# Kernel optimization log

Measured on AMD Instinct MI355X. Metric: run time of the kernel, lower is better.

The kernel has to match this reference:

```python
import jax, jax.numpy as jnp
import numpy as np

EPS = 1e-8  # torch F.cosine_similarity default eps


def setup_inputs() -> dict:
    key = jax.random.key(0)
    k1, k2, k3, k4 = jax.random.split(key, 4)
    U, I, L = 8192, 8192, 256
    # xavier_uniform bound for Embedding weight (fan_in=n, fan_out=L)
    bu = float(np.sqrt(6.0 / (U + L)))
    bi = float(np.sqrt(6.0 / (I + L)))
    user_embed_w = jax.random.uniform(k1, (U, L), jnp.float32, -bu, bu)
    item_embed_w = jax.random.uniform(k2, (I, L), jnp.float32, -bi, bi)
    user_idx = jax.random.randint(k3, (1024,), 0, U, dtype=jnp.int64 if jax.config.jax_enable_x64 else jnp.int32)
    item_idx = jax.random.randint(k4, (1024,), 0, I, dtype=jnp.int64 if jax.config.jax_enable_x64 else jnp.int32)
    return {
        "user_embed_w": user_embed_w,
        "item_embed_w": item_embed_w,
        "user_idx": user_idx,
        "item_idx": item_idx,
        "is_test": 1,
    }


def _cosine_full(u, v):
    # Faithful to F.cosine_similarity(u[:,None], v[None,:], dim=-1) but
    # expressed as normalize + GEMM: (u.v) / (max(|u|,eps)*max(|v|,eps)).
    un = u / jnp.maximum(jnp.linalg.norm(u, axis=-1, keepdims=True), EPS)
    vn = v / jnp.maximum(jnp.linalg.norm(v, axis=-1, keepdims=True), EPS)
    return jnp.einsum("ul,il->ui", un, vn)  # [U, I]


def reference(user_embed_w, item_embed_w, user_idx, item_idx, is_test):
    if is_test:
        return _cosine_full(user_embed_w, item_embed_w)
    # training path: per-pair cosine similarity of user embeddings (note:
    # original code looks up BOTH indices in user_embed, faithfully kept)
    a = user_embed_w[user_idx]
    b = user_embed_w[item_idx]
    num = jnp.sum(a * b, axis=-1)
    den = jnp.maximum(jnp.linalg.norm(a, axis=-1), EPS) * jnp.maximum(
        jnp.linalg.norm(b, axis=-1), EPS
    )
    return (num / den).reshape(-1, 1)
```

## Files before the change

kernel.cpp:

```cpp
#include <hip/hip_runtime.h>
#include <hip/hip_bf16.h>
#include <stdint.h>


#define LDIM 256
#define NROWS 8192
#define NDIM 8192
#define BM 128
#define BN 128
#define BK 64

typedef __bf16 bf16x8 __attribute__((ext_vector_type(8)));
typedef float f32x4 __attribute__((ext_vector_type(4)));

__device__ __forceinline__ unsigned short f2bf_rne(float f) {
  union { float f; uint32_t u; } c;
  c.f = f;
  uint32_t u = c.u;
  u += 0x7FFFu + ((u >> 16) & 1u);
  return (unsigned short)(u >> 16);
}

__global__ __launch_bounds__(256) void normalize_both(
    const float* __restrict__ userw, const float* __restrict__ itemw,
    unsigned short* __restrict__ dst) {
  const int wave = threadIdx.x >> 6;
  const int lane = threadIdx.x & 63;
  const int row = blockIdx.x * 4 + wave;
  const float* src = (row < NROWS)
                         ? userw + (size_t)row * LDIM
                         : itemw + (size_t)(row - NROWS) * LDIM;

  const float4 v = reinterpret_cast<const float4*>(src)[lane];
  float ss = v.x * v.x + v.y * v.y + v.z * v.z + v.w * v.w;
#pragma unroll
  for (int off = 32; off; off >>= 1) ss += __shfl_xor(ss, off, 64);
  const float rn = 1.0f / fmaxf(sqrtf(ss), 1e-8f);

  ushort4 o;
  o.x = f2bf_rne(v.x * rn);
  o.y = f2bf_rne(v.y * rn);
  o.z = f2bf_rne(v.z * rn);
  o.w = f2bf_rne(v.w * rn);
  reinterpret_cast<ushort4*>(dst + (size_t)row * LDIM)[lane] = o;
}

__device__ __forceinline__ void gld_lds16(const __bf16* g, __bf16* l) {
  __builtin_amdgcn_global_load_lds(
      (const __attribute__((address_space(1))) uint32_t*)g,
      (__attribute__((address_space(3))) uint32_t*)l, 16, 0, 0);
}

__global__ __launch_bounds__(256) void cos_gemm(
    const __bf16* __restrict__ A, const __bf16* __restrict__ B,
    float* __restrict__ C) {
  __shared__ __align__(16) __bf16 As[2][BM * BK];
  __shared__ __align__(16) __bf16 Bs[2][BN * BK];

  const int tid = threadIdx.x;
  const int wid = tid >> 6;
  const int lane = tid & 63;
  const int bn = blockIdx.x, bm = blockIdx.y;
  const int wr = wid >> 1, wc = wid & 1;

  const int srow = tid >> 3;
  const int scbx = (((tid & 7) ^ (srow & 7)) << 4);
  const __bf16* gA = A + (size_t)(bm * BM + srow) * LDIM + (scbx >> 1);
  const __bf16* gB = B + (size_t)(bn * BN + srow) * LDIM + (scbx >> 1);

  const int fr = lane & 15;
  const int q = lane >> 4;
  const int rsw = (fr & 7) << 4;

  f32x4 acc[4][4] = {};

#define STAGE(buf, kt)                                                       \
  {                                                                          \
    _Pragma("unroll") for (int c = 0; c < 4; ++c) {                          \
      gld_lds16(gA + (size_t)(c * 32) * LDIM + (kt)*BK,                      \
                &As[buf][c * 2048 + wid * 512]);                             \
      gld_lds16(gB + (size_t)(c * 32) * LDIM + (kt)*BK,                      \
                &Bs[buf][c * 2048 + wid * 512]);                             \
    }                                                                        \
  }

#define COMPUTE(buf)                                                         \
  {                                                                          \
    _Pragma("unroll") for (int ks = 0; ks < 2; ++ks) {                       \
      bf16x8 af[4], bv[4];                                                   \
      const int kb = ((((ks << 6) | (q << 4)) ^ rsw) >> 1);                  \
      _Pragma("unroll") for (int m = 0; m < 4; ++m)                          \
          af[m] = *reinterpret_cast<const bf16x8*>(                          \
              &As[buf][(wr * 64 + m * 16 + fr) * BK + kb]);                  \
      _Pragma("unroll") for (int n = 0; n < 4; ++n)                          \
          bv[n] = *reinterpret_cast<const bf16x8*>(                          \
              &Bs[buf][(wc * 64 + n * 16 + fr) * BK + kb]);                  \
      _Pragma("unroll") for (int m = 0; m < 4; ++m)                          \
          _Pragma("unroll") for (int n = 0; n < 4; ++n)                      \
              acc[m][n] = __builtin_amdgcn_mfma_f32_16x16x32_bf16(           \
                  bv[n], af[m], acc[m][n], 0, 0, 0);                         \
    }                                                                        \
  }

  STAGE(0, 0);
  __syncthreads();
#pragma unroll
  for (int kt = 0; kt < 3; ++kt) {
    STAGE((kt + 1) & 1, kt + 1);
    COMPUTE(kt & 1);
    __syncthreads();
  }
  COMPUTE(1);

  float* Cp = C + (size_t)(bm * BM + wr * 64 + fr) * NDIM +
              (bn * BN + wc * 64 + (q << 2));
#pragma unroll
  for (int m = 0; m < 4; ++m)
#pragma unroll
    for (int n = 0; n < 4; ++n)
      *reinterpret_cast<f32x4*>(Cp + (size_t)(m * 16) * NDIM + n * 16) =
          acc[m][n];
#undef STAGE
#undef COMPUTE
}

extern "C" void kernel_launch(void* const* d_in, const int* in_sizes, int n_in,
                              void* d_out, int out_size, void* d_ws, size_t ws_size,
                              hipStream_t stream) {
  const float* user_w = (const float*)d_in[0];
  const float* item_w = (const float*)d_in[1];
  float* out = (float*)d_out;

  unsigned short* un = (unsigned short*)d_ws;
  unsigned short* vn = un + (size_t)NROWS * LDIM;

  normalize_both<<<(2 * NROWS) / 4, 256, 0, stream>>>(user_w, item_w, un);

  dim3 grid(NDIM / BN, NDIM / BM);
  cos_gemm<<<grid, 256, 0, stream>>>((const __bf16*)un, (const __bf16*)vn, out);
}
```

Before: 82.88 us.

## Write normalized operands in MFMA fragment order and load directly to registers

The normalize kernel now stores bf16 rows in a pre-swizzled layout matching the 16x16x32 MFMA fragment order. The GEMM then drops LDS staging and barriers and loads fragments straight from global memory into registers with a two-deep register double buffer. This removes LDS traffic and sync overhead. In exchange, operand reuse within a block now depends on L1/L2 caching instead of shared memory, and vector register pressure goes up.

```diff
diff --git a/kernel.cpp b/kernel.cpp
--- a/kernel.cpp
+++ b/kernel.cpp
@@ -8,7 +8,6 @@
 #define NDIM 8192
 #define BM 128
 #define BN 128
-#define BK 64
 
 typedef __bf16 bf16x8 __attribute__((ext_vector_type(8)));
 typedef float f32x4 __attribute__((ext_vector_type(4)));
@@ -21,7 +20,7 @@
   return (unsigned short)(u >> 16);
 }
 
-__global__ __launch_bounds__(256) void normalize_both(
+__global__ __launch_bounds__(256) void normalize_frag(
     const float* __restrict__ userw, const float* __restrict__ itemw,
     unsigned short* __restrict__ dst) {
   const int wave = threadIdx.x >> 6;
@@ -42,76 +41,58 @@
   o.y = f2bf_rne(v.y * rn);
   o.z = f2bf_rne(v.z * rn);
   o.w = f2bf_rne(v.w * rn);
-  reinterpret_cast<ushort4*>(dst + (size_t)row * LDIM)[lane] = o;
-}
 
-__device__ __forceinline__ void gld_lds16(const __bf16* g, __bf16* l) {
-  __builtin_amdgcn_global_load_lds(
-      (const __attribute__((address_space(1))) uint32_t*)g,
-      (__attribute__((address_space(3))) uint32_t*)l, 16, 0, 0);
+  const size_t base = (row < NROWS ? 0 : (size_t)NROWS * LDIM) +
+                      (size_t)((row & 8191) >> 4) * 4096;
+  const size_t off = base + ((lane >> 3) << 9) + (((lane >> 1) & 3) << 7) +
+                     ((row & 15) << 3) + ((lane & 1) << 2);
+  *reinterpret_cast<ushort4*>(dst + off) = o;
 }
 
 __global__ __launch_bounds__(256) void cos_gemm(
     const __bf16* __restrict__ A, const __bf16* __restrict__ B,
     float* __restrict__ C) {
-  __shared__ __align__(16) __bf16 As[2][BM * BK];
-  __shared__ __align__(16) __bf16 Bs[2][BN * BK];
-
   const int tid = threadIdx.x;
   const int wid = tid >> 6;
   const int lane = tid & 63;
   const int bn = blockIdx.x, bm = blockIdx.y;
   const int wr = wid >> 1, wc = wid & 1;
 
-  const int srow = tid >> 3;
-  const int scbx = (((tid & 7) ^ (srow & 7)) << 4);
-  const __bf16* gA = A + (size_t)(bm * BM + srow) * LDIM + (scbx >> 1);
-  const __bf16* gB = B + (size_t)(bn * BN + srow) * LDIM + (scbx >> 1);
-
-  const int fr = lane & 15;
-  const int q = lane >> 4;
-  const int rsw = (fr & 7) << 4;
+  const bf16x8* pa =
+      reinterpret_cast<const bf16x8*>(A) + (size_t)(bm * 8 + wr * 4) * 512 + lane;
+  const bf16x8* pb =
+      reinterpret_cast<const bf16x8*>(B) + (size_t)(bn * 8 + wc * 4) * 512 + lane;
 
   f32x4 acc[4][4] = {};
+  bf16x8 a0[4], b0[4], a1[4], b1[4];
 
-#define STAGE(buf, kt)                                                       \
+#define LD(aa, bb, kt)                                                       \
   {                                                                          \
-    _Pragma("unroll") for (int c = 0; c < 4; ++c) {                          \
-      gld_lds16(gA + (size_t)(c * 32) * LDIM + (kt)*BK,                      \
-                &As[buf][c * 2048 + wid * 512]);                             \
-      gld_lds16(gB + (size_t)(c * 32) * LDIM + (kt)*BK,                      \
-                &Bs[buf][c * 2048 + wid * 512]);                             \
-    }                                                                        \
+    _Pragma("unroll") for (int m = 0; m < 4; ++m) aa[m] =                    \
+        pa[m * 512 + (kt)*64];                                               \
+    _Pragma("unroll") for (int n = 0; n < 4; ++n) bb[n] =                    \
+        pb[n * 512 + (kt)*64];                                               \
+  }
+#define STEP(aa, bb)                                                         \
+  {                                                                          \
+    _Pragma("unroll") for (int m = 0; m < 4; ++m)                            \
+        _Pragma("unroll") for (int n = 0; n < 4; ++n)                        \
+            acc[m][n] = __builtin_amdgcn_mfma_f32_16x16x32_bf16(             \
+                bb[n], aa[m], acc[m][n], 0, 0, 0);                           \
   }
 
-#define COMPUTE(buf)                                                         \
-  {                                                                          \
-    _Pragma("unroll") for (int ks = 0; ks < 2; ++ks) {                       \
-      bf16x8 af[4], bv[4];                                                   \
-      const int kb = ((((ks << 6) | (q << 4)) ^ rsw) >> 1);                  \
-      _Pragma("unroll") for (int m = 0; m < 4; ++m)                          \
-          af[m] = *reinterpret_cast<const bf16x8*>(                          \
-              &As[buf][(wr * 64 + m * 16 + fr) * BK + kb]);                  \
-      _Pragma("unroll") for (int n = 0; n < 4; ++n)                          \
-          bv[n] = *reinterpret_cast<const bf16x8*>(                          \
-              &Bs[buf][(wc * 64 + n * 16 + fr) * BK + kb]);                  \
-      _Pragma("unroll") for (int m = 0; m < 4; ++m)                          \
-          _Pragma("unroll") for (int n = 0; n < 4; ++n)                      \
-              acc[m][n] = __builtin_amdgcn_mfma_f32_16x16x32_bf16(           \
-                  bv[n], af[m], acc[m][n], 0, 0, 0);                         \
-    }                                                                        \
+  LD(a0, b0, 0);
+#pragma unroll
+  for (int kt = 0; kt < 8; kt += 2) {
+    if (kt + 1 < 8) LD(a1, b1, kt + 1);
+    STEP(a0, b0);
+    if (kt + 2 < 8) LD(a0, b0, kt + 2);
+    STEP(a1, b1);
   }
+#undef LD
+#undef STEP
 
-  STAGE(0, 0);
-  __syncthreads();
-#pragma unroll
-  for (int kt = 0; kt < 3; ++kt) {
-    STAGE((kt + 1) & 1, kt + 1);
-    COMPUTE(kt & 1);
-    __syncthreads();
-  }
-  COMPUTE(1);
-
+  const int fr = lane & 15, q = lane >> 4;
   float* Cp = C + (size_t)(bm * BM + wr * 64 + fr) * NDIM +
               (bn * BN + wc * 64 + (q << 2));
 #pragma unroll
@@ -120,8 +101,6 @@
     for (int n = 0; n < 4; ++n)
       *reinterpret_cast<f32x4*>(Cp + (size_t)(m * 16) * NDIM + n * 16) =
           acc[m][n];
-#undef STAGE
-#undef COMPUTE
 }
 
 extern "C" void kernel_launch(void* const* d_in, const int* in_sizes, int n_in,
@@ -134,7 +113,7 @@
   unsigned short* un = (unsigned short*)d_ws;
   unsigned short* vn = un + (size_t)NROWS * LDIM;
 
-  normalize_both<<<(2 * NROWS) / 4, 256, 0, stream>>>(user_w, item_w, un);
+  normalize_frag<<<(2 * NROWS) / 4, 256, 0, stream>>>(user_w, item_w, un);
 
   dim3 grid(NDIM / BN, NDIM / BM);
   cos_gemm<<<grid, 256, 0, stream>>>((const __bf16*)un, (const __bf16*)vn, out);
```

After: 92.48 us. 1.12x slower.

## Make GEMM blocks persistent over four N tiles with cross-tile prefetch pipeline

Applied to the files above, without the earlier changes.

Each block now computes four consecutive 128x128 output tiles along N, using BK=32 double-buffered stages. The first K-slice of the next tile is prefetched during the last slice of the current one, so stores overlap loads. Waits use explicit vmcnt counters instead of __syncthreads, and the grid drops to 1024 blocks. This cuts launch and prologue cost per tile and overlaps epilogue stores with loads. In exchange there are fewer blocks for the CUs, an unswizzled LDS layout with possible bank conflicts, and fragile hand-written vmcnt counts.

```diff
diff --git a/kernel.cpp b/kernel.cpp
--- a/kernel.cpp
+++ b/kernel.cpp
@@ -8,7 +8,8 @@
 #define NDIM 8192
 #define BM 128
 #define BN 128
-#define BK 64
+#define BK 32
+#define TPB 4
 
 typedef __bf16 bf16x8 __attribute__((ext_vector_type(8)));
 typedef float f32x4 __attribute__((ext_vector_type(4)));
@@ -54,72 +55,91 @@
 __global__ __launch_bounds__(256) void cos_gemm(
     const __bf16* __restrict__ A, const __bf16* __restrict__ B,
     float* __restrict__ C) {
-  __shared__ __align__(16) __bf16 As[2][BM * BK];
-  __shared__ __align__(16) __bf16 Bs[2][BN * BK];
+  __shared__ __bf16 As[2][BM * BK];
+  __shared__ __bf16 Bs[2][BN * BK];
 
   const int tid = threadIdx.x;
   const int wid = tid >> 6;
   const int lane = tid & 63;
-  const int bn = blockIdx.x, bm = blockIdx.y;
+  const int b = blockIdx.x;
+  const int bm = b >> 4;
+  const int bn0 = (b & 15) * TPB;
+
   const int wr = wid >> 1, wc = wid & 1;
 
-  const int srow = tid >> 3;
-  const int scbx = (((tid & 7) ^ (srow & 7)) << 4);
-  const __bf16* gA = A + (size_t)(bm * BM + srow) * LDIM + (scbx >> 1);
-  const __bf16* gB = B + (size_t)(bn * BN + srow) * LDIM + (scbx >> 1);
+  const int m0 = (wid << 5) + (lane >> 2);
+  const int k0 = (lane & 3) << 3;
+  const __bf16* gA = A + (size_t)(bm * BM + m0) * LDIM + k0;
+  const __bf16* gB = B + (size_t)(bn0 * BN + m0) * LDIM + k0;
 
   const int fr = lane & 15;
   const int q = lane >> 4;
-  const int rsw = (fr & 7) << 4;
+  const int kq = q << 3;
 
   f32x4 acc[4][4] = {};
 
-#define STAGE(buf, kt)                                                       \
+#define STAGE(buf, ko, gBp)                                                  \
   {                                                                          \
-    _Pragma("unroll") for (int c = 0; c < 4; ++c) {                          \
-      gld_lds16(gA + (size_t)(c * 32) * LDIM + (kt)*BK,                      \
-                &As[buf][c * 2048 + wid * 512]);                             \
-      gld_lds16(gB + (size_t)(c * 32) * LDIM + (kt)*BK,                      \
-                &Bs[buf][c * 2048 + wid * 512]);                             \
+    _Pragma("unroll") for (int c = 0; c < 2; ++c) {                          \
+      gld_lds16(gA + (size_t)(c * 16) * LDIM + (ko),                         \
+                &As[buf][(wid << 10) + (c << 9)]);                           \
+      gld_lds16((gBp) + (size_t)(c * 16) * LDIM + (ko),                      \
+                &Bs[buf][(wid << 10) + (c << 9)]);                           \
     }                                                                        \
   }
 
 #define COMPUTE(buf)                                                         \
   {                                                                          \
-    _Pragma("unroll") for (int ks = 0; ks < 2; ++ks) {                       \
-      bf16x8 af[4], bv[4];                                                   \
-      const int kb = ((((ks << 6) | (q << 4)) ^ rsw) >> 1);                  \
-      _Pragma("unroll") for (int m = 0; m < 4; ++m)                          \
-          af[m] = *reinterpret_cast<const bf16x8*>(                          \
-              &As[buf][(wr * 64 + m * 16 + fr) * BK + kb]);                  \
-      _Pragma("unroll") for (int n = 0; n < 4; ++n)                          \
-          bv[n] = *reinterpret_cast<const bf16x8*>(                          \
-              &Bs[buf][(wc * 64 + n * 16 + fr) * BK + kb]);                  \
-      _Pragma("unroll") for (int m = 0; m < 4; ++m)                          \
-          _Pragma("unroll") for (int n = 0; n < 4; ++n)                      \
-              acc[m][n] = __builtin_amdgcn_mfma_f32_16x16x32_bf16(           \
-                  bv[n], af[m], acc[m][n], 0, 0, 0);                         \
-    }                                                                        \
+    bf16x8 af[4], bv[4];                                                     \
+    _Pragma("unroll") for (int m = 0; m < 4; ++m)                            \
+        af[m] = *reinterpret_cast<const bf16x8*>(                            \
+            &As[buf][(wr * 64 + m * 16 + fr) * BK + kq]);                    \
+    _Pragma("unroll") for (int n = 0; n < 4; ++n)                            \
+        bv[n] = *reinterpret_cast<const bf16x8*>(                            \
+            &Bs[buf][(wc * 64 + n * 16 + fr) * BK + kq]);                    \
+    _Pragma("unroll") for (int m = 0; m < 4; ++m)                            \
+        _Pragma("unroll") for (int n = 0; n < 4; ++n)                        \
+            acc[m][n] = __builtin_amdgcn_mfma_f32_16x16x32_bf16(             \
+                bv[n], af[m], acc[m][n], 0, 0, 0);                           \
   }
 
-  STAGE(0, 0);
-  __syncthreads();
+  STAGE(0, 0, gB);
+  float* Cp = C + (size_t)(bm * BM + wr * 64 + fr) * NDIM +
+              (bn0 * BN + wc * 64 + (q << 2));
+
+  for (int t = 0; t < TPB; ++t) {
+    const __bf16* gBn = (t < TPB - 1) ? gB + (size_t)BN * LDIM : gB;
 #pragma unroll
-  for (int kt = 0; kt < 3; ++kt) {
-    STAGE((kt + 1) & 1, kt + 1);
-    COMPUTE(kt & 1);
-    __syncthreads();
+    for (int kt = 0; kt < 8; ++kt) {
+      const int buf = kt & 1;
+      if (kt < 7) STAGE(buf ^ 1, (kt + 1) * BK, gB)
+      else        STAGE(buf ^ 1, 0, gBn)
+      if (kt == 0 && t > 0) {
+        asm volatile("s_waitcnt vmcnt(20)" ::: "memory");
+      } else {
+        asm volatile("s_waitcnt vmcnt(4)" ::: "memory");
+      }
+      __builtin_amdgcn_s_barrier();
+      __builtin_amdgcn_sched_barrier(0);
+      COMPUTE(buf);
+      if (kt == 7) {
+#pragma unroll
+        for (int m = 0; m < 4; ++m)
+#pragma unroll
+          for (int n = 0; n < 4; ++n)
+            *reinterpret_cast<f32x4*>(Cp + (size_t)(m * 16) * NDIM + n * 16) =
+                acc[m][n];
+#pragma unroll
+        for (int m = 0; m < 4; ++m)
+#pragma unroll
+          for (int n = 0; n < 4; ++n) acc[m][n] = (f32x4)(0.0f);
+        Cp += BN;
+      }
+      __builtin_amdgcn_sched_barrier(0);
+      __builtin_amdgcn_s_barrier();
+    }
+    gB += (size_t)BN * LDIM;
   }
-  COMPUTE(1);
-
-  float* Cp = C + (size_t)(bm * BM + wr * 64 + fr) * NDIM +
-              (bn * BN + wc * 64 + (q << 2));
-#pragma unroll
-  for (int m = 0; m < 4; ++m)
-#pragma unroll
-    for (int n = 0; n < 4; ++n)
-      *reinterpret_cast<f32x4*>(Cp + (size_t)(m * 16) * NDIM + n * 16) =
-          acc[m][n];
 #undef STAGE
 #undef COMPUTE
 }
@@ -136,6 +156,5 @@
 
   normalize_both<<<(2 * NROWS) / 4, 256, 0, stream>>>(user_w, item_w, un);
 
-  dim3 grid(NDIM / BN, NDIM / BM);
-  cos_gemm<<<grid, 256, 0, stream>>>((const __bf16*)un, (const __bf16*)vn, out);
+  cos_gemm<<<1024, 256, 0, stream>>>((const __bf16*)un, (const __bf16*)vn, out);
 }
```

After: 93.74 us. 13.1% more time.
